# Performance work log

Hardware: AMD Instinct MI355X
Metric: run time of the kernel (lower is better)

Reference implementation:

```python
import jax, jax.numpy as jnp
import numpy as np

N_NODES = 100000
HIDDEN = 64
N_REL = 9
N_LAYERS = 3
N_EDGES = 1000000


def setup_inputs() -> dict:
    key = jax.random.key(0)
    k1, k2, k3, k4, k5 = jax.random.split(key, 5)
    edge_index = jax.random.randint(k1, (2, N_EDGES), 0, N_NODES, dtype=jnp.int64)
    edge_type = jax.random.randint(k2, (N_EDGES,), 0, N_REL, dtype=jnp.int64)
    embeddings = jax.random.uniform(k3, (N_NODES, HIDDEN), dtype=jnp.float32)
    weights = jax.random.uniform(k4, (N_LAYERS, 2 * N_REL, HIDDEN, HIDDEN), dtype=jnp.float32)
    biases = jax.random.uniform(k5, (N_LAYERS, 2 * N_REL, HIDDEN), dtype=jnp.float32)
    return {"edge_index": edge_index, "edge_type": edge_type,
            "embeddings": embeddings, "weights": weights, "biases": biases}


def reference(edge_index, edge_type, embeddings, weights, biases):
    # Faithful translation of RGCNEncoder.forward.
    # NOTE (faithful to source): get_messages always reads self.embeddings,
    # and both `sources` and `dests` are edge_index[d][edge_type == r].
    N, E = embeddings.shape
    L = weights.shape[0]
    R = weights.shape[1] // 2
    idx0 = edge_index[0]          # indices for direction d=0 (source == dest)
    idx1 = edge_index[1]          # indices for direction d=1
    rel0 = edge_type              # weight row r + R*0
    rel1 = edge_type + R          # weight row r + R*1

    output = embeddings
    for l in range(L):
        # Transform every node under every (relation, direction) weight once,
        # then gather per edge. Equivalent to per-relation gather->matmul, but
        # avoids materializing per-edge [E,E] weight matrices.
        T = jnp.einsum('ne,reo->rno', embeddings, weights[l])   # [2R, N, E]
        m0 = T[rel0, idx0] + biases[l][rel0]                    # [n_edges, E]
        m1 = T[rel1, idx1] + biases[l][rel1]                    # [n_edges, E]
        m = jnp.concatenate([m0, m1], axis=0)
        d = jnp.concatenate([idx0, idx1], axis=0)
        # scatter_mean over destination nodes (0 for nodes with no messages)
        s = jax.ops.segment_sum(m, d, num_segments=N)
        cnt = jax.ops.segment_sum(jnp.ones((d.shape[0],), m.dtype), d, num_segments=N)
        hidden = jnp.where(cnt[:, None] > 0, s / jnp.maximum(cnt, 1.0)[:, None], 0.0)
        if l + 1 < L:
            hidden = jax.nn.relu(hidden)
        output = hidden
    return output
```

## Files before the change

### kernel.cpp

```cpp
#include <hip/hip_runtime.h>


typedef float  floatx4 __attribute__((ext_vector_type(4)));
typedef short  shortx8 __attribute__((ext_vector_type(8)));
typedef unsigned int uint;
typedef unsigned char uchar;

#define MFMA_BF16(A, B, C) __builtin_amdgcn_mfma_f32_16x16x32_bf16((A), (B), (C), 0, 0, 0)

#define NBUF 512
#define NBKT 512
#define CAP  48
#define PREP_BLOCKS 296

static __device__ __forceinline__ ushort f32_to_bf16_rne(float f) {
    union { float f; unsigned u; } v; v.f = f;
    unsigned r = v.u + 0x7fffu + ((v.u >> 16) & 1u);
    return (ushort)(r >> 16);
}

static __device__ __forceinline__ void prep_item(
    int i, const float* __restrict__ w2, const float* __restrict__ b2,
    ushort* __restrict__ wt_sw, ushort* __restrict__ bias_sw)
{
    const int WELEMS = 18 * 8 * 64 * 8;
    if (i < WELEMS) {
        int r    = i >> 12;
        int rem  = i & 4095;
        int cid  = rem >> 9;
        int lane = (rem >> 3) & 63;
        int j    = i & 7;
        int nt = cid >> 1, kh = cid & 1;
        int o = nt * 16 + (lane & 15);
        int k = kh * 32 + (lane >> 4) * 8 + j;
        wt_sw[i] = f32_to_bf16_rne(w2[(r << 12) + (k << 6) + o]);
    } else {
        int i2 = i - WELEMS;
        if (i2 < 2048) {
            int nt   = i2 >> 9;
            int lane = (i2 >> 3) & 63;
            int j    = i2 & 7;
            int o  = nt * 16 + (lane & 15);
            int rr = (lane >> 4) * 8 + j;
            bias_sw[i2] = (rr < 18) ? f32_to_bf16_rne(b2[rr * 64 + o]) : (ushort)0;
        }
    }
}

__global__ __launch_bounds__(256) void rgcn_scatter_prep(
    const int*   __restrict__ ei,
    const int*   __restrict__ et,
    const float* __restrict__ w2,
    const float* __restrict__ b2,
    ushort*      __restrict__ cnt_tab,
    ushort*      __restrict__ data,
    ushort*      __restrict__ wt_sw,
    ushort*      __restrict__ bias_sw,
    int E, int N)
{
    __shared__ uint   cur[NBKT];
    __shared__ ushort bins[NBKT][CAP];

    const int t = threadIdx.x;

    if (blockIdx.x >= NBUF) {
        int i = (blockIdx.x - NBUF) * 256 + t;
        prep_item(i, w2, b2, wt_sw, bias_sw);
        return;
    }

    #pragma unroll
    for (int b = t; b < NBKT; b += 256) cur[b] = 0;
    __syncthreads();

    const int epb = (E + NBUF - 1) / NBUF;
    const int e0 = blockIdx.x * epb;
    const int e1 = (e0 + epb < E) ? e0 + epb : E;

    for (int e = e0 + t; e < e1; e += 256) {
        int r = et[e]; int i0 = ei[e]; int i1 = ei[E + e];
        if ((unsigned)r < 9u) {
            if ((unsigned)i0 < (unsigned)N) {
                int b = i0 >> 8;
                uint o = atomicAdd(&cur[b], 1u);
                if (o < CAP) bins[b][o] = (ushort)((i0 & 255) * 18 + r);
            }
            if ((unsigned)i1 < (unsigned)N) {
                int b = i1 >> 8;
                uint o = atomicAdd(&cur[b], 1u);
                if (o < CAP) bins[b][o] = (ushort)((i1 & 255) * 18 + 9 + r);
            }
        }
    }
    __syncthreads();

    const int blk = blockIdx.x;
    for (int b = t; b < NBKT; b += 256) {
        uint c = cur[b];
        if (c > CAP) c = CAP;
        cnt_tab[(size_t)blk * NBKT + b] = (ushort)c;
        uint words = (c + 1) >> 1;
        uint* dst = (uint*)(data + ((size_t)b * NBUF + blk) * CAP);
        const uint* srcp = (const uint*)&bins[b][0];
        for (uint wd = 0; wd < words; wd++) dst[wd] = srcp[wd];
    }
}

__global__ void rgcn_prep_k(const float* __restrict__ w2, const float* __restrict__ b2,
                            ushort* __restrict__ wt_sw, ushort* __restrict__ bias_sw) {
    prep_item(blockIdx.x * 256 + threadIdx.x, w2, b2, wt_sw, bias_sw);
}
__global__ void rgcn_count32(const int* __restrict__ ei, const int* __restrict__ et,
                             int* __restrict__ cnts, int E, int N) {
    int e = blockIdx.x * 256 + threadIdx.x;
    if (e < E) {
        int r = et[e];
        int i0 = ei[e];
        int i1 = ei[E + e];
        if ((unsigned)r < 9u) {
            if ((unsigned)i0 < (unsigned)N) atomicAdd(&cnts[i0 * 18 + r], 1);
            if ((unsigned)i1 < (unsigned)N) atomicAdd(&cnts[i1 * 18 + 9 + r], 1);
        }
    }
}
__global__ void rgcn_cvt8(const int* __restrict__ c32, uchar* __restrict__ c8, int total4) {
    int i = blockIdx.x * 256 + threadIdx.x;
    if (i < total4) {
        uint v = 0;
        #pragma unroll
        for (int j = 0; j < 4; j++) {
            int c = c32[i * 4 + j];
            if (c > 255) c = 255;
            v |= ((uint)c) << (8 * j);
        }
        ((uint*)c8)[i] = v;
    }
}

static __device__ __forceinline__ void load_af(
    const float* __restrict__ emb, int n, int q, shortx8 af[2])
{
    const float* rp = emb + (size_t)n * 64 + q * 8;
    #pragma unroll
    for (int kh = 0; kh < 2; kh++) {
        floatx4 lo = *(const floatx4*)(rp + kh * 32);
        floatx4 hi = *(const floatx4*)(rp + kh * 32 + 4);
        shortx8 f;
        #pragma unroll
        for (int j = 0; j < 4; j++) {
            f[j]     = (short)f32_to_bf16_rne(lo[j]);
            f[j + 4] = (short)f32_to_bf16_rne(hi[j]);
        }
        af[kh] = f;
    }
}

static __device__ __forceinline__ void gemm_store(
    const shortx8 af[4][2],
    const float  (*__restrict__ wft)[256],
    const ushort (*__restrict__ wbL)[32],
    const ushort* __restrict__ wbase,
    const ushort* __restrict__ bias_sw,
    float* __restrict__ out, int N,
    int lrow, int rowbase, int m, int q, int lane)
{
    shortx8 bA[8], bB[8];
    #pragma unroll
    for (int c = 0; c < 8; c++) bA[c] = *(const shortx8*)(wbase + c * 512);

    floatx4 acc[4][4];
    #pragma unroll
    for (int mt = 0; mt < 4; mt++)
        #pragma unroll
        for (int nt = 0; nt < 4; nt++)
            acc[mt][nt] = (floatx4){0.f, 0.f, 0.f, 0.f};

    for (int r = 0; r < 18; r += 2) {
        {
            const ushort* p = wbase + (size_t)(r + 1) * 4096;
            #pragma unroll
            for (int c = 0; c < 8; c++) bB[c] = *(const shortx8*)(p + c * 512);
        }
        {
            floatx4 swv[4];
            #pragma unroll
            for (int mt = 0; mt < 4; mt++)
                swv[mt] = *(const floatx4*)&wft[r][lrow + mt * 16 + q * 4];
            #pragma unroll
            for (int nt = 0; nt < 4; nt++)
                #pragma unroll
                for (int mt = 0; mt < 4; mt++) {
                    floatx4 tmp = (floatx4){0.f, 0.f, 0.f, 0.f};
                    tmp = MFMA_BF16(af[mt][0], bA[nt * 2 + 0], tmp);
                    tmp = MFMA_BF16(af[mt][1], bA[nt * 2 + 1], tmp);
                    acc[mt][nt] += swv[mt] * tmp;
                }
        }
        if (r + 2 < 18) {
            const ushort* p = wbase + (size_t)(r + 2) * 4096;
            #pragma unroll
            for (int c = 0; c < 8; c++) bA[c] = *(const shortx8*)(p + c * 512);
        }
        {
            floatx4 swv[4];
            #pragma unroll
            for (int mt = 0; mt < 4; mt++)
                swv[mt] = *(const floatx4*)&wft[r + 1][lrow + mt * 16 + q * 4];
            #pragma unroll
            for (int nt = 0; nt < 4; nt++)
                #pragma unroll
                for (int mt = 0; mt < 4; mt++) {
                    floatx4 tmp = (floatx4){0.f, 0.f, 0.f, 0.f};
                    tmp = MFMA_BF16(af[mt][0], bB[nt * 2 + 0], tmp);
                    tmp = MFMA_BF16(af[mt][1], bB[nt * 2 + 1], tmp);
                    acc[mt][nt] += swv[mt] * tmp;
                }
        }
    }

    #pragma unroll
    for (int nt = 0; nt < 4; nt++) {
        shortx8 btf = *(const shortx8*)(bias_sw + ((size_t)nt * 64 + lane) * 8);
        #pragma unroll
        for (int mt = 0; mt < 4; mt++) {
            shortx8 wfrag = *(const shortx8*)&wbL[lrow + mt * 16 + m][q * 8];
            acc[mt][nt] = MFMA_BF16(wfrag, btf, acc[mt][nt]);
        }
    }

    #pragma unroll
    for (int mt = 0; mt < 4; mt++)
        #pragma unroll
        for (int i = 0; i < 4; i++) {
            int nn = rowbase + mt * 16 + q * 4 + i;
            if (nn < N) {
                #pragma unroll
                for (int nt = 0; nt < 4; nt++)
                    out[(size_t)nn * 64 + nt * 16 + m] = acc[mt][nt][i];
            }
        }
}

__global__ __launch_bounds__(256, 2) void rgcn_main(
    const float*  __restrict__ emb,
    const ushort* __restrict__ cnt_tab,
    const ushort* __restrict__ data,
    const ushort* __restrict__ wt_sw,
    const ushort* __restrict__ bias_sw,
    float*        __restrict__ out,
    int N)
{
    __shared__ int    cnt[4608];
    __shared__ float  wft[18][256];
    __shared__ ushort wbL[256][32];
    __shared__ ushort scnt[NBUF];

    const int t    = threadIdx.x;
    const int b    = blockIdx.x;
    const int wave = t >> 6;
    const int lane = t & 63;
    const int m    = lane & 15;
    const int q    = lane >> 4;
    const int rowbase = b * 256 + wave * 64;
    const int lrow    = wave * 64;

    #pragma unroll
    for (int i = t; i < 4608; i += 256) cnt[i] = 0;
    #pragma unroll
    for (int w = t; w < NBUF; w += 256) scnt[w] = cnt_tab[(size_t)w * NBKT + b];

    shortx8 af[4][2];
    #pragma unroll
    for (int mt = 0; mt < 4; mt++) {
        int n = rowbase + mt * 16 + m;
        if (n >= N) n = N - 1;
        load_af(emb, n, q, af[mt]);
    }
    const ushort* wbase = wt_sw + (size_t)lane * 8;

    __syncthreads();

    #pragma unroll
    for (int w = t; w < NBUF; w += 256) {
        uint c = scnt[w];
        const ushort* seg = data + ((size_t)b * NBUF + w) * CAP;
        for (uint i = 0; i < c; i++) atomicAdd(&cnt[seg[i]], 1);
    }
    __syncthreads();

    {
        int c[18]; int s = 0;
        #pragma unroll
        for (int r = 0; r < 18; r++) { c[r] = cnt[t * 18 + r]; s += c[r]; }
        float inv = (s > 0) ? (1.0f / (float)s) : 0.0f;
        #pragma unroll
        for (int r = 0; r < 18; r++) {
            float w = (float)c[r] * inv;
            wft[r][t] = w;
            wbL[t][r] = f32_to_bf16_rne(w);
        }
        #pragma unroll
        for (int r = 18; r < 32; r++) wbL[t][r] = 0;
    }
    __syncthreads();

    gemm_store(af, wft, wbL, wbase, bias_sw, out, N, lrow, rowbase, m, q, lane);
}

__global__ __launch_bounds__(256, 2) void rgcn_main_c8(
    const float*  __restrict__ emb,
    const uchar*  __restrict__ cnts8,
    const ushort* __restrict__ wt_sw,
    const ushort* __restrict__ bias_sw,
    float*        __restrict__ out,
    int N)
{
    __shared__ float  wft[18][256];
    __shared__ ushort wbL[256][32];
    __shared__ uchar  craw[4608];

    const int t    = threadIdx.x;
    const int wave = t >> 6;
    const int lane = t & 63;
    const int m    = lane & 15;
    const int q    = lane >> 4;
    const int rowbase = blockIdx.x * 256 + wave * 64;
    const int lrow    = wave * 64;

    {
        const uint* srcp = (const uint*)(cnts8 + (size_t)blockIdx.x * 4608);
        uint* d = (uint*)craw;
        #pragma unroll
        for (int i = t; i < 1152; i += 256) d[i] = srcp[i];
    }
    shortx8 af[4][2];
    #pragma unroll
    for (int mt = 0; mt < 4; mt++) {
        int n = rowbase + mt * 16 + m;
        if (n >= N) n = N - 1;
        load_af(emb, n, q, af[mt]);
    }
    const ushort* wbase = wt_sw + (size_t)lane * 8;
    __syncthreads();
    {
        int c[18]; int s = 0;
        const uchar* cp = &craw[t * 18];
        #pragma unroll
        for (int r = 0; r < 18; r++) { c[r] = cp[r]; s += c[r]; }
        float inv = (s > 0) ? (1.0f / (float)s) : 0.0f;
        #pragma unroll
        for (int r = 0; r < 18; r++) {
            float w = (float)c[r] * inv;
            wft[r][t] = w;
            wbL[t][r] = f32_to_bf16_rne(w);
        }
        #pragma unroll
        for (int r = 18; r < 32; r++) wbL[t][r] = 0;
    }
    __syncthreads();
    gemm_store(af, wft, wbL, wbase, bias_sw, out, N, lrow, rowbase, m, q, lane);
}

extern "C" void kernel_launch(void* const* d_in, const int* in_sizes, int n_in,
                              void* d_out, int out_size, void* d_ws, size_t ws_size,
                              hipStream_t stream) {
    const int*   edge_index = (const int*)d_in[0];
    const int*   edge_type  = (const int*)d_in[1];
    const float* emb        = (const float*)d_in[2];
    const float* weights    = (const float*)d_in[3];
    const float* biases     = (const float*)d_in[4];
    float* out = (float*)d_out;

    const int E = in_sizes[1];
    const int N = in_sizes[2] / 64;
    const int nbuckets = (N + 255) >> 8;

    const float* w2 = weights + 2 * 18 * 64 * 64;
    const float* b2 = biases  + 2 * 18 * 64;

    size_t off = 0;
    auto take = [&](size_t bytes) { void* p = (char*)d_ws + off; off = (off + bytes + 63) & ~(size_t)63; return p; };
    ushort* cnt_tab = (ushort*)take((size_t)NBUF * NBKT * 2);
    ushort* data    = (ushort*)take((size_t)NBKT * NBUF * CAP * 2);
    ushort* wt_sw   = (ushort*)take(73728 * 2);
    ushort* bias_sw = (ushort*)take(2048 * 2);
    size_t need = off;

    if (ws_size >= need && nbuckets <= NBKT) {
        rgcn_scatter_prep<<<NBUF + PREP_BLOCKS, 256, 0, stream>>>(
            edge_index, edge_type, w2, b2, cnt_tab, data, wt_sw, bias_sw, E, N);
        rgcn_main<<<nbuckets, 256, 0, stream>>>(
            emb, cnt_tab, data, wt_sw, bias_sw, out, N);
    } else {
        int* c32 = (int*)d_ws;
        uchar* cnts8 = (uchar*)((char*)d_ws + (((size_t)nbuckets * 4608 * 4 + 63) & ~(size_t)63));
        wt_sw   = (ushort*)(cnts8 + (size_t)nbuckets * 4608);
        bias_sw = wt_sw + 73728;
        rgcn_prep_k<<<PREP_BLOCKS, 256, 0, stream>>>(w2, b2, wt_sw, bias_sw);
        hipMemsetAsync(c32, 0, (size_t)nbuckets * 4608 * 4, stream);
        rgcn_count32<<<(E + 255) / 256, 256, 0, stream>>>(edge_index, edge_type, c32, E, N);
        int total4 = nbuckets * 4608 / 4;
        rgcn_cvt8<<<(total4 + 255) / 256, 256, 0, stream>>>(c32, cnts8, total4);
        rgcn_main_c8<<<nbuckets, 256, 0, stream>>>(emb, cnts8, wt_sw, bias_sw, out, N);
    }
}
```

Before: 125.2 us.

## Stage weight swizzle through LDS, transpose count table, add per-iteration barrier

The weight-prep blocks in the scatter kernel now load each relation's 64x64 fp32 weight matrix coalesced into shared memory and then write the swizzled bf16 layout, using 19 blocks instead of 296 strided-gather blocks. The per-bucket count table is transposed to bucket-major so the main kernel reads its 512 counts contiguously. A workgroup barrier is inserted at the top of each relation-pair iteration in the MFMA loop, likely to keep the waves in step on the shared weight loads. The barrier adds synchronisation cost, and fewer prep blocks means less parallelism for that part of the work.

```diff
diff --git a/kernel.cpp b/kernel.cpp
--- a/kernel.cpp
+++ b/kernel.cpp
@@ -11,7 +11,7 @@
 #define NBUF 512
 #define NBKT 512
 #define CAP  48
-#define PREP_BLOCKS 296
+#define PREPB 19
 
 static __device__ __forceinline__ ushort f32_to_bf16_rne(float f) {
     union { float f; unsigned u; } v; v.f = f;
@@ -19,10 +19,99 @@
     return (ushort)(r >> 16);
 }
 
-static __device__ __forceinline__ void prep_item(
-    int i, const float* __restrict__ w2, const float* __restrict__ b2,
-    ushort* __restrict__ wt_sw, ushort* __restrict__ bias_sw)
+__global__ __launch_bounds__(256) void rgcn_scatter_prep(
+    const int*   __restrict__ ei,
+    const int*   __restrict__ et,
+    const float* __restrict__ w2,
+    const float* __restrict__ b2,
+    ushort*      __restrict__ cnt_tab,
+    ushort*      __restrict__ data,
+    ushort*      __restrict__ wt_sw,
+    ushort*      __restrict__ bias_sw,
+    int E, int N)
 {
+    __shared__ uint   cur[NBKT];
+    __shared__ ushort bins[NBKT][CAP];
+
+    const int t = threadIdx.x;
+
+    if (blockIdx.x >= NBUF) {
+        int pb = blockIdx.x - NBUF;
+        ushort* wlds = &bins[0][0];
+        if (pb < 18) {
+            const float* src = w2 + (pb << 12);
+            #pragma unroll
+            for (int i = 0; i < 16; i++) {
+                int idx = t + 256 * i;
+                wlds[idx] = f32_to_bf16_rne(src[idx]);
+            }
+            __syncthreads();
+            ushort* dst = wt_sw + (pb << 12);
+            #pragma unroll
+            for (int u = 0; u < 16; u++) {
+                int d = t * 16 + u;
+                int cid  = d >> 9;
+                int lane = (d >> 3) & 63;
+                int j    = d & 7;
+                int o = (cid >> 1) * 16 + (lane & 15);
+                int k = (cid & 1) * 32 + (lane >> 4) * 8 + j;
+                dst[d] = wlds[(k << 6) + o];
+            }
+        } else {
+            #pragma unroll
+            for (int u = 0; u < 8; u++) {
+                int i2 = t * 8 + u;
+                int nt   = i2 >> 9;
+                int lane = (i2 >> 3) & 63;
+                int j    = i2 & 7;
+                int o  = nt * 16 + (lane & 15);
+                int rr = (lane >> 4) * 8 + j;
+                bias_sw[i2] = (rr < 18) ? f32_to_bf16_rne(b2[rr * 64 + o]) : (ushort)0;
+            }
+        }
+        return;
+    }
+
+    #pragma unroll
+    for (int b = t; b < NBKT; b += 256) cur[b] = 0;
+    __syncthreads();
+
+    const int epb = (E + NBUF - 1) / NBUF;
+    const int e0 = blockIdx.x * epb;
+    const int e1 = (e0 + epb < E) ? e0 + epb : E;
+
+    for (int e = e0 + t; e < e1; e += 256) {
+        int r = et[e]; int i0 = ei[e]; int i1 = ei[E + e];
+        if ((unsigned)r < 9u) {
+            if ((unsigned)i0 < (unsigned)N) {
+                int b = i0 >> 8;
+                uint o = atomicAdd(&cur[b], 1u);
+                if (o < CAP) bins[b][o] = (ushort)((i0 & 255) * 18 + r);
+            }
+            if ((unsigned)i1 < (unsigned)N) {
+                int b = i1 >> 8;
+                uint o = atomicAdd(&cur[b], 1u);
+                if (o < CAP) bins[b][o] = (ushort)((i1 & 255) * 18 + 9 + r);
+            }
+        }
+    }
+    __syncthreads();
+
+    const int blk = blockIdx.x;
+    for (int b = t; b < NBKT; b += 256) {
+        uint c = cur[b];
+        if (c > CAP) c = CAP;
+        cnt_tab[(size_t)b * NBUF + blk] = (ushort)c;
+        uint words = (c + 1) >> 1;
+        uint* dst = (uint*)(data + ((size_t)b * NBUF + blk) * CAP);
+        const uint* srcp = (const uint*)&bins[b][0];
+        for (uint wd = 0; wd < words; wd++) dst[wd] = srcp[wd];
+    }
+}
+
+__global__ void rgcn_prep_k(const float* __restrict__ w2, const float* __restrict__ b2,
+                            ushort* __restrict__ wt_sw, ushort* __restrict__ bias_sw) {
+    int i = blockIdx.x * 256 + threadIdx.x;
     const int WELEMS = 18 * 8 * 64 * 8;
     if (i < WELEMS) {
         int r    = i >> 12;
@@ -46,70 +135,6 @@
         }
     }
 }
-
-__global__ __launch_bounds__(256) void rgcn_scatter_prep(
-    const int*   __restrict__ ei,
-    const int*   __restrict__ et,
-    const float* __restrict__ w2,
-    const float* __restrict__ b2,
-    ushort*      __restrict__ cnt_tab,
-    ushort*      __restrict__ data,
-    ushort*      __restrict__ wt_sw,
-    ushort*      __restrict__ bias_sw,
-    int E, int N)
-{
-    __shared__ uint   cur[NBKT];
-    __shared__ ushort bins[NBKT][CAP];
-
-    const int t = threadIdx.x;
-
-    if (blockIdx.x >= NBUF) {
-        int i = (blockIdx.x - NBUF) * 256 + t;
-        prep_item(i, w2, b2, wt_sw, bias_sw);
-        return;
-    }
-
-    #pragma unroll
-    for (int b = t; b < NBKT; b += 256) cur[b] = 0;
-    __syncthreads();
-
-    const int epb = (E + NBUF - 1) / NBUF;
-    const int e0 = blockIdx.x * epb;
-    const int e1 = (e0 + epb < E) ? e0 + epb : E;
-
-    for (int e = e0 + t; e < e1; e += 256) {
-        int r = et[e]; int i0 = ei[e]; int i1 = ei[E + e];
-        if ((unsigned)r < 9u) {
-            if ((unsigned)i0 < (unsigned)N) {
-                int b = i0 >> 8;
-                uint o = atomicAdd(&cur[b], 1u);
-                if (o < CAP) bins[b][o] = (ushort)((i0 & 255) * 18 + r);
-            }
-            if ((unsigned)i1 < (unsigned)N) {
-                int b = i1 >> 8;
-                uint o = atomicAdd(&cur[b], 1u);
-                if (o < CAP) bins[b][o] = (ushort)((i1 & 255) * 18 + 9 + r);
-            }
-        }
-    }
-    __syncthreads();
-
-    const int blk = blockIdx.x;
-    for (int b = t; b < NBKT; b += 256) {
-        uint c = cur[b];
-        if (c > CAP) c = CAP;
-        cnt_tab[(size_t)blk * NBKT + b] = (ushort)c;
-        uint words = (c + 1) >> 1;
-        uint* dst = (uint*)(data + ((size_t)b * NBUF + blk) * CAP);
-        const uint* srcp = (const uint*)&bins[b][0];
-        for (uint wd = 0; wd < words; wd++) dst[wd] = srcp[wd];
-    }
-}
-
-__global__ void rgcn_prep_k(const float* __restrict__ w2, const float* __restrict__ b2,
-                            ushort* __restrict__ wt_sw, ushort* __restrict__ bias_sw) {
-    prep_item(blockIdx.x * 256 + threadIdx.x, w2, b2, wt_sw, bias_sw);
-}
 __global__ void rgcn_count32(const int* __restrict__ ei, const int* __restrict__ et,
                              int* __restrict__ cnts, int E, int N) {
     int e = blockIdx.x * 256 + threadIdx.x;
@@ -176,6 +201,7 @@
             acc[mt][nt] = (floatx4){0.f, 0.f, 0.f, 0.f};
 
     for (int r = 0; r < 18; r += 2) {
+        __builtin_amdgcn_s_barrier();
         {
             const ushort* p = wbase + (size_t)(r + 1) * 4096;
             #pragma unroll
@@ -267,7 +293,7 @@
     #pragma unroll
     for (int i = t; i < 4608; i += 256) cnt[i] = 0;
     #pragma unroll
-    for (int w = t; w < NBUF; w += 256) scnt[w] = cnt_tab[(size_t)w * NBKT + b];
+    for (int w = t; w < NBUF; w += 256) scnt[w] = cnt_tab[(size_t)b * NBUF + w];
 
     shortx8 af[4][2];
     #pragma unroll
@@ -380,14 +406,14 @@
 
     size_t off = 0;
     auto take = [&](size_t bytes) { void* p = (char*)d_ws + off; off = (off + bytes + 63) & ~(size_t)63; return p; };
-    ushort* cnt_tab = (ushort*)take((size_t)NBUF * NBKT * 2);
+    ushort* cnt_tab = (ushort*)take((size_t)NBKT * NBUF * 2);
     ushort* data    = (ushort*)take((size_t)NBKT * NBUF * CAP * 2);
     ushort* wt_sw   = (ushort*)take(73728 * 2);
     ushort* bias_sw = (ushort*)take(2048 * 2);
     size_t need = off;
 
     if (ws_size >= need && nbuckets <= NBKT) {
-        rgcn_scatter_prep<<<NBUF + PREP_BLOCKS, 256, 0, stream>>>(
+        rgcn_scatter_prep<<<NBUF + PREPB, 256, 0, stream>>>(
             edge_index, edge_type, w2, b2, cnt_tab, data, wt_sw, bias_sw, E, N);
         rgcn_main<<<nbuckets, 256, 0, stream>>>(
             emb, cnt_tab, data, wt_sw, bias_sw, out, N);
@@ -396,7 +422,7 @@
         uchar* cnts8 = (uchar*)((char*)d_ws + (((size_t)nbuckets * 4608 * 4 + 63) & ~(size_t)63));
         wt_sw   = (ushort*)(cnts8 + (size_t)nbuckets * 4608);
         bias_sw = wt_sw + 73728;
-        rgcn_prep_k<<<PREP_BLOCKS, 256, 0, stream>>>(w2, b2, wt_sw, bias_sw);
+        rgcn_prep_k<<<(73728 + 2048 + 255) / 256, 256, 0, stream>>>(w2, b2, wt_sw, bias_sw);
         hipMemsetAsync(c32, 0, (size_t)nbuckets * 4608 * 4, stream);
         rgcn_count32<<<(E + 255) / 256, 256, 0, stream>>>(edge_index, edge_type, c32, E, N);
         int total4 = nbuckets * 4608 / 4;
```

Result: no change. 124.5 us (-0.5%).
